# Kernel tuning notes

Measured on AMD Instinct MI355X. Metric: run time of the kernel, lower is better.

The kernel has to match this reference:

```python
import jax, jax.numpy as jnp
import numpy as np
from jax import lax

B, N, C = 32, 4096, 512
HEADS, K, U = 4, 16, 4
V = C // HEADS  # 128
KS = 7
EPS = 1e-3  # keras LayerNormalization default epsilon


def _layernorm(x, g, b):
    mu = jnp.mean(x, axis=-1, keepdims=True)
    var = jnp.var(x, axis=-1, keepdims=True)
    return (x - mu) * lax.rsqrt(var + EPS) * g + b


def setup_inputs() -> dict:
    key = jax.random.key(0)
    ks = jax.random.split(key, 6)
    sc = lambda fan: 1.0 / np.sqrt(fan)
    x = jax.random.normal(ks[0], (B, N, C), dtype=jnp.float32)
    wq = jax.random.normal(ks[1], (C, K * HEADS), dtype=jnp.float32) * sc(C)
    wk = jax.random.normal(ks[2], (C, K * U), dtype=jnp.float32) * sc(C)
    wv = jax.random.normal(ks[3], (C, V * U), dtype=jnp.float32) * sc(C)
    gq = jnp.ones((K * HEADS,), jnp.float32)
    bq = jnp.zeros((K * HEADS,), jnp.float32)
    gv = jnp.ones((V * U,), jnp.float32)
    bv = jnp.zeros((V * U,), jnp.float32)
    pos_w = jax.random.normal(ks[4], (1, KS, U, K), dtype=jnp.float32) * sc(KS * U)
    pos_b = jnp.zeros((K,), jnp.float32)
    return {"x": x, "wq": wq, "wk": wk, "wv": wv, "gq": gq, "bq": bq,
            "gv": gv, "bv": bv, "pos_w": pos_w, "pos_b": pos_b}


def reference(x, wq, wk, wv, gq, bq, gv, bv, pos_w, pos_b):
    # 1x1 conv projections == per-position matmuls
    q = _layernorm(x @ wq, gq, bq)                      # (B, N, K*HEADS)
    k = x @ wk                                          # (B, N, K*U)
    v = _layernorm(x @ wv, gv, bv)                      # (B, N, V*U)
    # rearranges (Reshape + Permute((2,3,1)))
    q = q.reshape(B, N, HEADS, K).transpose(0, 2, 3, 1)  # (B, H, K, N)
    k = k.reshape(B, N, U, K).transpose(0, 2, 3, 1)      # (B, U, K, N)
    v = v.reshape(B, N, U, V).transpose(0, 2, 3, 1)      # (B, U, V, N)
    k = jax.nn.softmax(k, axis=-1)                       # softmax over positions n
    # content lambda
    lc = jnp.einsum('bukn,buvn->bkv', k, v)              # (B, K, V)
    yc = jnp.einsum('bhkn,bkv->bnhv', q, lc)             # (B, N, H, V)
    # positional lambda: Conv2D(K, (1, KS), 'same') over (B, V, N, U) NHWC
    v2 = v.transpose(0, 2, 3, 1)                         # (B, V, N, U)
    lp = lax.conv_general_dilated(v2, pos_w, (1, 1), 'SAME',
                                  dimension_numbers=('NHWC', 'HWIO', 'NHWC')) + pos_b  # (B, V, N, K)
    lp = lp.transpose(0, 1, 3, 2)                        # (B, V, K, N)
    yp = jnp.einsum('bhkn,bvkn->bnhv', q, lp)            # (B, N, H, V)
    return (yc + yp).reshape(B, N, HEADS * V)            # (B, N, out_dim)
```

## Files before the change

kernel.cpp:

```cpp
#include <hip/hip_runtime.h>
#include <hip/hip_bf16.h>


#define Bb   32
#define Nn   4096
#define Cc   512
#define Hh   4
#define Kk   16
#define Uu   4
#define Vv   128
#define QKVW 640
#define MTOT (Bb*Nn)
#define EPSf 1e-3f

typedef __bf16 bf16;
typedef bf16  bf16x8 __attribute__((ext_vector_type(8)));
typedef bf16  bf16x4 __attribute__((ext_vector_type(4)));
typedef float f32x4  __attribute__((ext_vector_type(4)));

#define WT_OFF   0UL
#define QKV_OFF  655360UL
#define QMU_OFF  168427520UL
#define QRS_OFF  168951808UL
#define VMU_OFF  169476096UL
#define VRS_OFF  170000384UL
#define KPM_OFF  170524672UL
#define KPS_OFF  170590208UL
#define KMX_OFF  170655744UL
#define KIV_OFF  170663936UL
#define LCP_OFF  170672128UL
#define LC_OFF   174866432UL

__device__ inline float bf2f(bf16 x) { return (float)x; }

__global__ __launch_bounds__(256) void k0_weights(
    const float* __restrict__ wq, const float* __restrict__ wk,
    const float* __restrict__ wv, bf16* __restrict__ wt)
{
    int idx = blockIdx.x * 256 + threadIdx.x;
    if (idx >= Cc * QKVW) return;
    int c = idx / QKVW, j = idx % QKVW;
    float v;
    if (j < 64)       v = wq[c * 64 + j];
    else if (j < 128) v = wk[c * 64 + (j - 64)];
    else              v = wv[c * 512 + (j - 128)];
    wt[(size_t)j * Cc + c] = (bf16)v;
}

__global__ __launch_bounds__(256) void k1_gemm(
    const float* __restrict__ x, const bf16* __restrict__ wt,
    bf16* __restrict__ qkv)
{
    int bid = blockIdx.x;
    int swz = (bid & 7) * 640 + (bid >> 3);
    int bm = swz / 5, bn = swz % 5;
    int row0 = bm * 128, col0 = bn * 128;

    int tid  = threadIdx.x;
    int lane = tid & 63, w = tid >> 6;
    int wr = (w >> 1) * 64, wc = (w & 1) * 64;
    int l15 = lane & 15, l4 = lane >> 4;

    __shared__ __align__(16) bf16 As[128 * 72];
    __shared__ __align__(16) bf16 Bs[128 * 72];

    f32x4 acc[4][4];
#pragma unroll
    for (int m = 0; m < 4; ++m)
#pragma unroll
        for (int c = 0; c < 4; ++c) { acc[m][c][0]=0.f; acc[m][c][1]=0.f; acc[m][c][2]=0.f; acc[m][c][3]=0.f; }

    const int srow = tid >> 3;
    const int schk = (tid & 7) * 8;

    for (int kt = 0; kt < 8; ++kt) {
        int kb = kt * 64;
        __syncthreads();
#pragma unroll
        for (int it = 0; it < 4; ++it) {
            int r = it * 32 + srow;
            const float* src = x + (size_t)(row0 + r) * Cc + kb + schk;
            f32x4 lo = *(const f32x4*)src;
            f32x4 hi = *(const f32x4*)(src + 4);
            bf16x8 pk;
            pk[0]=(bf16)lo[0]; pk[1]=(bf16)lo[1]; pk[2]=(bf16)lo[2]; pk[3]=(bf16)lo[3];
            pk[4]=(bf16)hi[0]; pk[5]=(bf16)hi[1]; pk[6]=(bf16)hi[2]; pk[7]=(bf16)hi[3];
            *(bf16x8*)&As[r * 72 + schk] = pk;
        }
#pragma unroll
        for (int it = 0; it < 4; ++it) {
            int cI = it * 32 + srow;
            bf16x8 bvv = *(const bf16x8*)(wt + (size_t)(col0 + cI) * Cc + kb + schk);
            *(bf16x8*)&Bs[cI * 72 + schk] = bvv;
        }
        __syncthreads();
#pragma unroll
        for (int kk = 0; kk < 2; ++kk) {
            int ko = kk * 32 + l4 * 8;
            bf16x8 aF[4], bF[4];
#pragma unroll
            for (int m = 0; m < 4; ++m)
                aF[m] = *(const bf16x8*)&As[(wr + 16 * m + l15) * 72 + ko];
#pragma unroll
            for (int c = 0; c < 4; ++c)
                bF[c] = *(const bf16x8*)&Bs[(wc + 16 * c + l15) * 72 + ko];
#pragma unroll
            for (int m = 0; m < 4; ++m)
#pragma unroll
                for (int c = 0; c < 4; ++c)
                    acc[m][c] = __builtin_amdgcn_mfma_f32_16x16x32_bf16(aF[m], bF[c], acc[m][c], 0, 0, 0);
        }
    }
#pragma unroll
    for (int m = 0; m < 4; ++m)
#pragma unroll
        for (int c = 0; c < 4; ++c) {
            int grow = row0 + wr + 16 * m + l4 * 4;
            int gcol = col0 + wc + 16 * c + l15;
#pragma unroll
            for (int r = 0; r < 4; ++r)
                qkv[(size_t)(grow + r) * QKVW + gcol] = (bf16)acc[m][c][r];
        }
}

__global__ __launch_bounds__(256) void k2a_kpart(
    const bf16* __restrict__ qkv, float* __restrict__ kpm, float* __restrict__ kps)
{
    int ns = blockIdx.x;
    int b  = blockIdx.y;
    int t  = threadIdx.x;
    int c0 = (t & 7) * 8;
    int stripe = t >> 3;
    float m[8], s[8];
#pragma unroll
    for (int j = 0; j < 8; ++j) { m[j] = -1e30f; s[j] = 0.f; }
    for (int i = 0; i < 16; ++i) {
        int n = ns * 512 + stripe + i * 32;
        bf16x8 kv = *(const bf16x8*)(qkv + (size_t)(b * Nn + n) * QKVW + 64 + c0);
#pragma unroll
        for (int j = 0; j < 8; ++j) {
            float f = bf2f(kv[j]);
            float mn = fmaxf(m[j], f);
            s[j] = s[j] * __expf(m[j] - mn) + __expf(f - mn);
            m[j] = mn;
        }
    }
    __shared__ float pm[64 * 32], ps[64 * 32];
#pragma unroll
    for (int j = 0; j < 8; ++j) { pm[(c0 + j) * 32 + stripe] = m[j]; ps[(c0 + j) * 32 + stripe] = s[j]; }
    __syncthreads();
    if (t < 64) {
        float M = -1e30f;
        for (int i = 0; i < 32; ++i) M = fmaxf(M, pm[t * 32 + i]);
        float S = 0.f;
        for (int i = 0; i < 32; ++i) S += ps[t * 32 + i] * __expf(pm[t * 32 + i] - M);
        kpm[(b * 8 + ns) * 64 + t] = M;
        kps[(b * 8 + ns) * 64 + t] = S;
    }
}

__global__ __launch_bounds__(256) void k2a2_kfinal(
    const float* __restrict__ kpm, const float* __restrict__ kps,
    float* __restrict__ kmax, float* __restrict__ kinv)
{
    int idx = blockIdx.x * 256 + threadIdx.x;
    if (idx >= 2048) return;
    int b = idx >> 6, c = idx & 63;
    float M = -1e30f;
#pragma unroll
    for (int ns = 0; ns < 8; ++ns) M = fmaxf(M, kpm[(b * 8 + ns) * 64 + c]);
    float S = 0.f;
#pragma unroll
    for (int ns = 0; ns < 8; ++ns) S += kps[(b * 8 + ns) * 64 + c] * __expf(kpm[(b * 8 + ns) * 64 + c] - M);
    kmax[idx] = M;
    kinv[idx] = 1.0f / S;
}

__global__ __launch_bounds__(256) void k2b_lnstats(
    const bf16* __restrict__ qkv, float* __restrict__ qmu, float* __restrict__ qrs,
    float* __restrict__ vmu, float* __restrict__ vrs)
{
    int row = blockIdx.x * 256 + threadIdx.x;
    const bf16* p = qkv + (size_t)row * QKVW;
    float s = 0.f, ss = 0.f;
#pragma unroll
    for (int i = 0; i < 8; ++i) {
        bf16x8 v = *(const bf16x8*)(p + i * 8);
#pragma unroll
        for (int j = 0; j < 8; ++j) { float f = bf2f(v[j]); s += f; ss += f * f; }
    }
    float mu = s * (1.f / 64.f);
    float var = ss * (1.f / 64.f) - mu * mu;
    qmu[row] = mu; qrs[row] = rsqrtf(var + EPSf);
    s = 0.f; ss = 0.f;
#pragma unroll
    for (int i = 0; i < 64; ++i) {
        bf16x8 v = *(const bf16x8*)(p + 128 + i * 8);
#pragma unroll
        for (int j = 0; j < 8; ++j) { float f = bf2f(v[j]); s += f; ss += f * f; }
    }
    mu = s * (1.f / 512.f);
    var = ss * (1.f / 512.f) - mu * mu;
    vmu[row] = mu; vrs[row] = rsqrtf(var + EPSf);
}

__global__ __launch_bounds__(256) void k3_lc(
    const bf16* __restrict__ qkv, const float* __restrict__ kmax, const float* __restrict__ kinv,
    const float* __restrict__ vmu, const float* __restrict__ vrs,
    const float* __restrict__ gv, const float* __restrict__ bv,
    float* __restrict__ lcp)
{
    int ns = blockIdx.x;
    int b  = blockIdx.y;
    int t  = threadIdx.x;

    __shared__ __align__(16) float vln[16 * 512];
    __shared__ float smk[16 * 64];
    __shared__ float gvl[512], bvl[512];
    for (int i = t; i < 512; i += 256) { gvl[i] = gv[i]; bvl[i] = bv[i]; }

    int kk = t >> 4, vg = t & 15;
    float acc[8];
#pragma unroll
    for (int j = 0; j < 8; ++j) acc[j] = 0.f;

    for (int ch = 0; ch < 16; ++ch) {
        int nb = ns * 256 + ch * 16;
        __syncthreads();
        {
            int c0  = (t & 63) * 8;
            int nl0 = t >> 6;
#pragma unroll
            for (int i = 0; i < 4; ++i) {
                int nl = nl0 + i * 4;
                int row = b * Nn + nb + nl;
                bf16x8 v8 = *(const bf16x8*)(qkv + (size_t)row * QKVW + 128 + c0);
                float mu = vmu[row], rs = vrs[row];
#pragma unroll
                for (int j = 0; j < 8; ++j)
                    vln[nl * 512 + c0 + j] = (bf2f(v8[j]) - mu) * rs * gvl[c0 + j] + bvl[c0 + j];
            }
        }
        {
            int c0 = (t & 15) * 4;
            int nl = t >> 4;
            int row = b * Nn + nb + nl;
            bf16x4 k4 = *(const bf16x4*)(qkv + (size_t)row * QKVW + 64 + c0);
#pragma unroll
            for (int j = 0; j < 4; ++j)
                smk[nl * 64 + c0 + j] = __expf(bf2f(k4[j]) - kmax[b * 64 + c0 + j]) * kinv[b * 64 + c0 + j];
        }
        __syncthreads();
#pragma unroll 4
        for (int nl = 0; nl < 16; ++nl) {
#pragma unroll
            for (int u = 0; u < 4; ++u) {
                float sm = smk[nl * 64 + u * 16 + kk];
                f32x4 a = *(const f32x4*)&vln[nl * 512 + u * 128 + vg * 8];
                f32x4 c = *(const f32x4*)&vln[nl * 512 + u * 128 + vg * 8 + 4];
                acc[0] += sm * a[0]; acc[1] += sm * a[1]; acc[2] += sm * a[2]; acc[3] += sm * a[3];
                acc[4] += sm * c[0]; acc[5] += sm * c[1]; acc[6] += sm * c[2]; acc[7] += sm * c[3];
            }
        }
    }
    float* dst = lcp + (size_t)(b * 16 + ns) * 2048 + kk * 128 + vg * 8;
#pragma unroll
    for (int j = 0; j < 8; ++j) dst[j] = acc[j];
}

__global__ __launch_bounds__(256) void k3b_lcreduce(
    const float* __restrict__ lcp, float* __restrict__ lc)
{
    int idx = blockIdx.x * 256 + threadIdx.x;
    int b = idx >> 11, cc = idx & 2047;
    float s = 0.f;
#pragma unroll
    for (int ns = 0; ns < 16; ++ns) s += lcp[(size_t)(b * 16 + ns) * 2048 + cc];
    lc[idx] = s;
}

__global__ __launch_bounds__(256) void k4_out(
    const bf16* __restrict__ qkv, const float* __restrict__ qmu, const float* __restrict__ qrs,
    const float* __restrict__ vmu, const float* __restrict__ vrs,
    const float* __restrict__ gq, const float* __restrict__ bq,
    const float* __restrict__ gv, const float* __restrict__ bv,
    const float* __restrict__ posw, const float* __restrict__ posb,
    const float* __restrict__ lc, float* __restrict__ out)
{
    int nt = blockIdx.x;
    int b  = blockIdx.y;
    int t  = threadIdx.x;
    int vv = t & 127, hp = t >> 7;
    int n0 = nt * 128;

    __shared__ __align__(16) float qln[32 * 64];
    __shared__ __align__(16) float rls[32 * 4 * 32];
    __shared__ __align__(16) float pw[448];
    __shared__ __align__(16) float pb[16];
    for (int i = t; i < 448; i += 256) pw[i] = posw[i];
    if (t < 16) pb[t] = posb[t];

    f32x4 lcr4[4];
#pragma unroll
    for (int g = 0; g < 4; ++g)
#pragma unroll
        for (int j = 0; j < 4; ++j)
            lcr4[g][j] = lc[b * 2048 + (g * 4 + j) * 128 + vv];
    f32x4 gvr, bvr;
#pragma unroll
    for (int u = 0; u < 4; ++u) { gvr[u] = gv[u * 128 + vv]; bvr[u] = bv[u * 128 + vv]; }

    auto loadrow = [&](int mrow) -> f32x4 {
        f32x4 r;
        if ((unsigned)mrow < (unsigned)Nn) {
            int row = b * Nn + mrow;
            float mu = vmu[row], rs = vrs[row];
            const bf16* pr = qkv + (size_t)row * QKVW + 128 + vv;
#pragma unroll
            for (int u = 0; u < 4; ++u)
                r[u] = (bf2f(pr[u * 128]) - mu) * rs * gvr[u] + bvr[u];
        } else {
            r[0] = 0.f; r[1] = 0.f; r[2] = 0.f; r[3] = 0.f;
        }
        return r;
    };

    f32x4 wnd[7];
#pragma unroll
    for (int kq = 0; kq < 6; ++kq) wnd[kq] = loadrow(n0 - 3 + kq);

    for (int chk = 0; chk < 4; ++chk) {
        int nb = n0 + chk * 32;
        __syncthreads();
        {
            int rl = t >> 3, c0 = (t & 7) * 8;
            int row = b * Nn + nb + rl;
            bf16x8 qv = *(const bf16x8*)(qkv + (size_t)row * QKVW + c0);
            float mu = qmu[row], rs = qrs[row];
#pragma unroll
            for (int j = 0; j < 8; ++j)
                qln[rl * 64 + c0 + j] = (bf2f(qv[j]) - mu) * rs * gq[c0 + j] + bq[c0 + j];
        }
        __syncthreads();
        {
            int rh = t & 127;
            int rl = rh >> 2, h = rh & 3;
            int half = t >> 7;
            f32x4 q0 = *(const f32x4*)&qln[rl * 64 + h * 16 + 0];
            f32x4 q1 = *(const f32x4*)&qln[rl * 64 + h * 16 + 4];
            f32x4 q2 = *(const f32x4*)&qln[rl * 64 + h * 16 + 8];
            f32x4 q3 = *(const f32x4*)&qln[rl * 64 + h * 16 + 12];
            int j0 = half ? 15 : 0, j1 = half ? 29 : 15;
            for (int j = j0; j < j1; ++j) {
                const float* ps = (j < 28) ? &pw[j * 16] : &pb[0];
                f32x4 p0 = *(const f32x4*)(ps + 0);
                f32x4 p1 = *(const f32x4*)(ps + 4);
                f32x4 p2 = *(const f32x4*)(ps + 8);
                f32x4 p3 = *(const f32x4*)(ps + 12);
                float d = q0[0]*p0[0] + q0[1]*p0[1] + q0[2]*p0[2] + q0[3]*p0[3]
                        + q1[0]*p1[0] + q1[1]*p1[1] + q1[2]*p1[2] + q1[3]*p1[3]
                        + q2[0]*p2[0] + q2[1]*p2[1] + q2[2]*p2[2] + q2[3]*p2[3]
                        + q3[0]*p3[0] + q3[1]*p3[1] + q3[2]*p3[2] + q3[3]*p3[3];
                rls[(rl * 4 + h) * 32 + j] = d;
            }
        }
        __syncthreads();
        for (int i = 0; i < 32; ++i) {
            int nn = nb + i;
            wnd[6] = loadrow(nn + 3);
#pragma unroll
            for (int hh = 0; hh < 2; ++hh) {
                int h = hp * 2 + hh;
                int rbase = (i * 4 + h) * 32;
                float acc = rls[rbase + 28];
                f32x4 qa = *(const f32x4*)&qln[i * 64 + h * 16 + 0];
                f32x4 qb = *(const f32x4*)&qln[i * 64 + h * 16 + 4];
                f32x4 qc = *(const f32x4*)&qln[i * 64 + h * 16 + 8];
                f32x4 qd = *(const f32x4*)&qln[i * 64 + h * 16 + 12];
#pragma unroll
                for (int j = 0; j < 4; ++j) acc += qa[j] * lcr4[0][j];
#pragma unroll
                for (int j = 0; j < 4; ++j) acc += qb[j] * lcr4[1][j];
#pragma unroll
                for (int j = 0; j < 4; ++j) acc += qc[j] * lcr4[2][j];
#pragma unroll
                for (int j = 0; j < 4; ++j) acc += qd[j] * lcr4[3][j];
#pragma unroll
                for (int d = 0; d < 7; ++d) {
                    f32x4 rr = *(const f32x4*)&rls[rbase + d * 4];
                    acc += rr[0] * wnd[d][0] + rr[1] * wnd[d][1]
                         + rr[2] * wnd[d][2] + rr[3] * wnd[d][3];
                }
                out[(size_t)(b * Nn + nn) * 512 + h * 128 + vv] = acc;
            }
            wnd[0] = wnd[1]; wnd[1] = wnd[2]; wnd[2] = wnd[3];
            wnd[3] = wnd[4]; wnd[4] = wnd[5]; wnd[5] = wnd[6];
        }
    }
}

extern "C" void kernel_launch(void* const* d_in, const int* in_sizes, int n_in,
                              void* d_out, int out_size, void* d_ws, size_t ws_size,
                              hipStream_t stream) {
    const float* x    = (const float*)d_in[0];
    const float* wq   = (const float*)d_in[1];
    const float* wk   = (const float*)d_in[2];
    const float* wv   = (const float*)d_in[3];
    const float* gq   = (const float*)d_in[4];
    const float* bq   = (const float*)d_in[5];
    const float* gv   = (const float*)d_in[6];
    const float* bv   = (const float*)d_in[7];
    const float* posw = (const float*)d_in[8];
    const float* posb = (const float*)d_in[9];
    float* out = (float*)d_out;

    char* ws = (char*)d_ws;
    bf16*  wt   = (bf16*)(ws + WT_OFF);
    bf16*  qkv  = (bf16*)(ws + QKV_OFF);
    float* qmu  = (float*)(ws + QMU_OFF);
    float* qrs  = (float*)(ws + QRS_OFF);
    float* vmu  = (float*)(ws + VMU_OFF);
    float* vrs  = (float*)(ws + VRS_OFF);
    float* kpm  = (float*)(ws + KPM_OFF);
    float* kps  = (float*)(ws + KPS_OFF);
    float* kmax = (float*)(ws + KMX_OFF);
    float* kinv = (float*)(ws + KIV_OFF);
    float* lcp  = (float*)(ws + LCP_OFF);
    float* lc   = (float*)(ws + LC_OFF);

    k0_weights<<<(Cc * QKVW + 255) / 256, 256, 0, stream>>>(wq, wk, wv, wt);
    k1_gemm<<<5120, 256, 0, stream>>>(x, wt, qkv);
    k2a_kpart<<<dim3(8, 32), 256, 0, stream>>>(qkv, kpm, kps);
    k2a2_kfinal<<<8, 256, 0, stream>>>(kpm, kps, kmax, kinv);
    k2b_lnstats<<<512, 256, 0, stream>>>(qkv, qmu, qrs, vmu, vrs);
    k3_lc<<<dim3(16, 32), 256, 0, stream>>>(qkv, kmax, kinv, vmu, vrs, gv, bv, lcp);
    k3b_lcreduce<<<256, 256, 0, stream>>>(lcp, lc);
    k4_out<<<dim3(32, 32), 256, 0, stream>>>(qkv, qmu, qrs, vmu, vrs, gq, bq, gv, bv,
                                             posw, posb, lc, out);
}
```

Measured before the change: 523.7 us.

## Recast output kernel as bf16 MFMA GEMMs over packed lambda panels

The output kernel is rewritten so each block handles 16 positions. It first computes q·pos_w with an MFMA, then evaluates both the content and positional lambda contributions as bf16 16x16x32 MFMAs over shared-memory panels. The panels hold lc, a bias column and the 7-tap windowed normalized v. This replaces the scalar FP32 dot-product loops and per-thread sliding-window loads, and uses a much larger grid. It adds bf16 rounding of q, lc and the intermediate q·pos products, which costs accuracy, and it redoes the window halo loads for every small tile.

```diff
diff --git a/kernel.cpp b/kernel.cpp
--- a/kernel.cpp
+++ b/kernel.cpp
@@ -10,7 +10,6 @@
 #define Uu   4
 #define Vv   128
 #define QKVW 640
-#define MTOT (Bb*Nn)
 #define EPSf 1e-3f
 
 typedef __bf16 bf16;
@@ -279,6 +278,10 @@
     lc[idx] = s;
 }
 
+#define TN4    16
+#define NPAN4  15
+#define PELEM  1056
+
 __global__ __launch_bounds__(256) void k4_out(
     const bf16* __restrict__ qkv, const float* __restrict__ qmu, const float* __restrict__ qrs,
     const float* __restrict__ vmu, const float* __restrict__ vrs,
@@ -287,114 +290,147 @@
     const float* __restrict__ posw, const float* __restrict__ posb,
     const float* __restrict__ lc, float* __restrict__ out)
 {
-    int nt = blockIdx.x;
-    int b  = blockIdx.y;
-    int t  = threadIdx.x;
-    int vv = t & 127, hp = t >> 7;
-    int n0 = nt * 128;
-
-    __shared__ __align__(16) float qln[32 * 64];
-    __shared__ __align__(16) float rls[32 * 4 * 32];
-    __shared__ __align__(16) float pw[448];
-    __shared__ __align__(16) float pb[16];
-    for (int i = t; i < 448; i += 256) pw[i] = posw[i];
-    if (t < 16) pb[t] = posb[t];
-
-    f32x4 lcr4[4];
-#pragma unroll
-    for (int g = 0; g < 4; ++g)
-#pragma unroll
-        for (int j = 0; j < 4; ++j)
-            lcr4[g][j] = lc[b * 2048 + (g * 4 + j) * 128 + vv];
-    f32x4 gvr, bvr;
-#pragma unroll
-    for (int u = 0; u < 4; ++u) { gvr[u] = gv[u * 128 + vv]; bvr[u] = bv[u * 128 + vv]; }
-
-    auto loadrow = [&](int mrow) -> f32x4 {
-        f32x4 r;
-        if ((unsigned)mrow < (unsigned)Nn) {
-            int row = b * Nn + mrow;
+    const int nt = blockIdx.x, b = blockIdx.y, t = threadIdx.x;
+    const int n0 = nt * TN4;
+
+    __shared__ __align__(16) bf16 PN[NPAN4 * PELEM];
+    __shared__ __align__(16) bf16 Ax[64 * 104];
+    __shared__ __align__(16) bf16 PP[4 * 256];
+
+    bf16x8 z8;
+#pragma unroll
+    for (int j = 0; j < 8; ++j) z8[j] = (bf16)0.f;
+    for (int i = t; i < 832; i += 256) *(bf16x8*)&Ax[i * 8] = z8;
+    if (t < 128) *(bf16x8*)&PP[t * 8] = z8;
+    __syncthreads();
+
+    if (t < 64) {
+        int g = t >> 5, du = t & 31;
+        if (du < 28) {
+            f32x4 a = *(const f32x4*)(posw + du * 16 + g * 8);
+            f32x4 c = *(const f32x4*)(posw + du * 16 + g * 8 + 4);
+            bf16x8 pk;
+            pk[0]=(bf16)a[0]; pk[1]=(bf16)a[1]; pk[2]=(bf16)a[2]; pk[3]=(bf16)a[3];
+            pk[4]=(bf16)c[0]; pk[5]=(bf16)c[1]; pk[6]=(bf16)c[2]; pk[7]=(bf16)c[3];
+            *(bf16x8*)&PP[g * 256 + du * 8] = pk;
+        }
+    }
+    {
+        int p = t >> 7, v = t & 127;
+        const float* src = lc + b * 2048 + p * 8 * 128 + v;
+        bf16x8 pk;
+#pragma unroll
+        for (int j = 0; j < 8; ++j) pk[j] = (bf16)src[j * 128];
+        *(bf16x8*)&PN[p * PELEM + v * 8] = pk;
+        if (t < 128) {
+            bf16x8 ones = z8; ones[0] = (bf16)1.0f;
+            *(bf16x8*)&PN[2 * PELEM + t * 8] = ones;
+            *(bf16x8*)&PN[3 * PELEM + t * 8] = z8;
+        }
+    }
+    for (int it = t; it < 22 * 16; it += 256) {
+        int lr = it >> 4, vo = it & 15;
+        int n  = n0 - 3 + lr;
+        int pbase = (4 + (lr >> 1)) * PELEM + (lr & 1) * 4;
+        if ((unsigned)n < (unsigned)Nn) {
+            int row = b * Nn + n;
             float mu = vmu[row], rs = vrs[row];
-            const bf16* pr = qkv + (size_t)row * QKVW + 128 + vv;
-#pragma unroll
-            for (int u = 0; u < 4; ++u)
-                r[u] = (bf2f(pr[u * 128]) - mu) * rs * gvr[u] + bvr[u];
+            float f[4][8];
+#pragma unroll
+            for (int u = 0; u < 4; ++u) {
+                bf16x8 v8 = *(const bf16x8*)(qkv + (size_t)row * QKVW + 128 + u * 128 + vo * 8);
+                f32x4 g0 = *(const f32x4*)(gv + u * 128 + vo * 8);
+                f32x4 g1 = *(const f32x4*)(gv + u * 128 + vo * 8 + 4);
+                f32x4 b0 = *(const f32x4*)(bv + u * 128 + vo * 8);
+                f32x4 b1 = *(const f32x4*)(bv + u * 128 + vo * 8 + 4);
+#pragma unroll
+                for (int j = 0; j < 4; ++j) f[u][j]     = (bf2f(v8[j])     - mu) * rs * g0[j] + b0[j];
+#pragma unroll
+                for (int j = 0; j < 4; ++j) f[u][4 + j] = (bf2f(v8[4 + j]) - mu) * rs * g1[j] + b1[j];
+            }
+#pragma unroll
+            for (int vi = 0; vi < 8; ++vi) {
+                bf16x4 pk;
+                pk[0]=(bf16)f[0][vi]; pk[1]=(bf16)f[1][vi]; pk[2]=(bf16)f[2][vi]; pk[3]=(bf16)f[3][vi];
+                *(bf16x4*)&PN[pbase + (vo * 8 + vi) * 8] = pk;
+            }
         } else {
-            r[0] = 0.f; r[1] = 0.f; r[2] = 0.f; r[3] = 0.f;
-        }
-        return r;
-    };
-
-    f32x4 wnd[7];
-#pragma unroll
-    for (int kq = 0; kq < 6; ++kq) wnd[kq] = loadrow(n0 - 3 + kq);
-
-    for (int chk = 0; chk < 4; ++chk) {
-        int nb = n0 + chk * 32;
-        __syncthreads();
-        {
-            int rl = t >> 3, c0 = (t & 7) * 8;
-            int row = b * Nn + nb + rl;
-            bf16x8 qv = *(const bf16x8*)(qkv + (size_t)row * QKVW + c0);
-            float mu = qmu[row], rs = qrs[row];
-#pragma unroll
-            for (int j = 0; j < 8; ++j)
-                qln[rl * 64 + c0 + j] = (bf2f(qv[j]) - mu) * rs * gq[c0 + j] + bq[c0 + j];
-        }
-        __syncthreads();
-        {
-            int rh = t & 127;
-            int rl = rh >> 2, h = rh & 3;
-            int half = t >> 7;
-            f32x4 q0 = *(const f32x4*)&qln[rl * 64 + h * 16 + 0];
-            f32x4 q1 = *(const f32x4*)&qln[rl * 64 + h * 16 + 4];
-            f32x4 q2 = *(const f32x4*)&qln[rl * 64 + h * 16 + 8];
-            f32x4 q3 = *(const f32x4*)&qln[rl * 64 + h * 16 + 12];
-            int j0 = half ? 15 : 0, j1 = half ? 29 : 15;
-            for (int j = j0; j < j1; ++j) {
-                const float* ps = (j < 28) ? &pw[j * 16] : &pb[0];
-                f32x4 p0 = *(const f32x4*)(ps + 0);
-                f32x4 p1 = *(const f32x4*)(ps + 4);
-                f32x4 p2 = *(const f32x4*)(ps + 8);
-                f32x4 p3 = *(const f32x4*)(ps + 12);
-                float d = q0[0]*p0[0] + q0[1]*p0[1] + q0[2]*p0[2] + q0[3]*p0[3]
-                        + q1[0]*p1[0] + q1[1]*p1[1] + q1[2]*p1[2] + q1[3]*p1[3]
-                        + q2[0]*p2[0] + q2[1]*p2[1] + q2[2]*p2[2] + q2[3]*p2[3]
-                        + q3[0]*p3[0] + q3[1]*p3[1] + q3[2]*p3[2] + q3[3]*p3[3];
-                rls[(rl * 4 + h) * 32 + j] = d;
-            }
-        }
-        __syncthreads();
-        for (int i = 0; i < 32; ++i) {
-            int nn = nb + i;
-            wnd[6] = loadrow(nn + 3);
-#pragma unroll
-            for (int hh = 0; hh < 2; ++hh) {
-                int h = hp * 2 + hh;
-                int rbase = (i * 4 + h) * 32;
-                float acc = rls[rbase + 28];
-                f32x4 qa = *(const f32x4*)&qln[i * 64 + h * 16 + 0];
-                f32x4 qb = *(const f32x4*)&qln[i * 64 + h * 16 + 4];
-                f32x4 qc = *(const f32x4*)&qln[i * 64 + h * 16 + 8];
-                f32x4 qd = *(const f32x4*)&qln[i * 64 + h * 16 + 12];
-#pragma unroll
-                for (int j = 0; j < 4; ++j) acc += qa[j] * lcr4[0][j];
-#pragma unroll
-                for (int j = 0; j < 4; ++j) acc += qb[j] * lcr4[1][j];
-#pragma unroll
-                for (int j = 0; j < 4; ++j) acc += qc[j] * lcr4[2][j];
-#pragma unroll
-                for (int j = 0; j < 4; ++j) acc += qd[j] * lcr4[3][j];
-#pragma unroll
-                for (int d = 0; d < 7; ++d) {
-                    f32x4 rr = *(const f32x4*)&rls[rbase + d * 4];
-                    acc += rr[0] * wnd[d][0] + rr[1] * wnd[d][1]
-                         + rr[2] * wnd[d][2] + rr[3] * wnd[d][3];
-                }
-                out[(size_t)(b * Nn + nn) * 512 + h * 128 + vv] = acc;
-            }
-            wnd[0] = wnd[1]; wnd[1] = wnd[2]; wnd[2] = wnd[3];
-            wnd[3] = wnd[4]; wnd[4] = wnd[5]; wnd[5] = wnd[6];
+            bf16x4 zz; zz[0]=(bf16)0.f; zz[1]=(bf16)0.f; zz[2]=(bf16)0.f; zz[3]=(bf16)0.f;
+#pragma unroll
+            for (int vi = 0; vi < 8; ++vi)
+                *(bf16x4*)&PN[pbase + (vo * 8 + vi) * 8] = zz;
+        }
+    }
+    if (t < 128) {
+        int row = t >> 1, half = t & 1;
+        int n = n0 + (row >> 2), h = row & 3;
+        int gr = b * Nn + n;
+        int c0 = h * 16 + half * 8;
+        bf16x8 q8 = *(const bf16x8*)(qkv + (size_t)gr * QKVW + c0);
+        float mu = qmu[gr], rs = qrs[gr];
+        f32x4 gg0 = *(const f32x4*)(gq + c0), gg1 = *(const f32x4*)(gq + c0 + 4);
+        f32x4 bb0 = *(const f32x4*)(bq + c0), bb1 = *(const f32x4*)(bq + c0 + 4);
+        f32x4 pb0 = *(const f32x4*)(posb + half * 8), pb1 = *(const f32x4*)(posb + half * 8 + 4);
+        float qbp = 0.f;
+        bf16x8 pk;
+#pragma unroll
+        for (int j = 0; j < 4; ++j) {
+            float f = (bf2f(q8[j]) - mu) * rs * gg0[j] + bb0[j];
+            qbp += f * pb0[j]; pk[j] = (bf16)f;
+        }
+#pragma unroll
+        for (int j = 0; j < 4; ++j) {
+            float f = (bf2f(q8[4 + j]) - mu) * rs * gg1[j] + bb1[j];
+            qbp += f * pb1[j]; pk[4 + j] = (bf16)f;
+        }
+        *(bf16x8*)&Ax[row * 104 + half * 8] = pk;
+        float qb = qbp + __shfl_xor(qbp, 1);
+        if (!half) Ax[row * 104 + 16] = (bf16)qb;
+    }
+    __syncthreads();
+
+    const int lane = t & 63, rt = t >> 6;
+    const int g = lane >> 4, l15 = lane & 15;
+    const int arow = rt * 16 + l15;
+
+    bf16x8 aF0 = *(const bf16x8*)&Ax[arow * 104 + g * 8];
+    f32x4 zf; zf[0]=0.f; zf[1]=0.f; zf[2]=0.f; zf[3]=0.f;
+#pragma unroll
+    for (int ct = 0; ct < 2; ++ct) {
+        bf16x8 bp = *(const bf16x8*)&PP[g * 256 + (ct * 16 + l15) * 8];
+        f32x4 rf = __builtin_amdgcn_mfma_f32_16x16x32_bf16(aF0, bp, zf, 0, 0, 0);
+        int du = ct * 16 + l15;
+#pragma unroll
+        for (int reg = 0; reg < 4; ++reg) {
+            int row = rt * 16 + g * 4 + reg;
+            Ax[row * 104 + 32 + g * 4 + du] = (bf16)rf[reg];
+        }
+    }
+
+    bf16x8 aF1 = *(const bf16x8*)&Ax[arow * 104 + 32 + g * 8];
+    bf16x8 aF2 = *(const bf16x8*)&Ax[arow * 104 + 64 + g * 8];
+    const int P1 = (4 + rt * 2 + g) * PELEM;
+    const int P2 = (4 + rt * 2 + 4) * PELEM;
+    f32x4 acc[8];
+#pragma unroll
+    for (int c = 0; c < 8; ++c) acc[c] = zf;
+#pragma unroll
+    for (int c = 0; c < 8; ++c) {
+        int vb = (c * 16 + l15) * 8;
+        bf16x8 b0 = *(const bf16x8*)&PN[g * PELEM + vb];
+        bf16x8 b1 = *(const bf16x8*)&PN[P1 + vb];
+        bf16x8 b2 = *(const bf16x8*)&PN[P2 + vb];
+        acc[c] = __builtin_amdgcn_mfma_f32_16x16x32_bf16(aF0, b0, acc[c], 0, 0, 0);
+        acc[c] = __builtin_amdgcn_mfma_f32_16x16x32_bf16(aF1, b1, acc[c], 0, 0, 0);
+        acc[c] = __builtin_amdgcn_mfma_f32_16x16x32_bf16(aF2, b2, acc[c], 0, 0, 0);
+    }
+#pragma unroll
+    for (int c = 0; c < 8; ++c) {
+#pragma unroll
+        for (int reg = 0; reg < 4; ++reg) {
+            int row = rt * 16 + g * 4 + reg;
+            int n = n0 + (row >> 2), h = row & 3;
+            out[((size_t)(b * Nn + n)) * 512 + h * 128 + c * 16 + l15] = acc[c][reg];
         }
     }
 }
@@ -435,6 +471,6 @@
     k2b_lnstats<<<512, 256, 0, stream>>>(qkv, qmu, qrs, vmu, vrs);
     k3_lc<<<dim3(16, 32), 256, 0, stream>>>(qkv, kmax, kinv, vmu, vrs, gv, bv, lcp);
     k3b_lcreduce<<<256, 256, 0, stream>>>(lcp, lc);
-    k4_out<<<dim3(32, 32), 256, 0, stream>>>(qkv, qmu, qrs, vmu, vrs, gq, bq, gv, bv,
-                                             posw, posb, lc, out);
-}
+    k4_out<<<dim3(Nn / TN4, Bb), 256, 0, stream>>>(qkv, qmu, qrs, vmu, vrs, gq, bq, gv, bv,
+                                                   posw, posb, lc, out);
+}
```

Result: faster. 438.7 us (-16.2%).
